# Kernel optimization log

Hardware: AMD Instinct MI355X
Metric: run time of the kernel (lower is better)

Reference implementation:

```python
import jax, jax.numpy as jnp
import numpy as np

LEVELS = 16
N_MIN = 16
N_MAX = 512
TABLE_SIZE = 524288  # 2**19, power of two -> mod == bitmask
INPUT_DIM = 2
FEATURE_DIM = 2
N_POINTS = 1048576

# geometric resolution schedule (matches torch __init__)
_b = np.exp((np.log(N_MAX) - np.log(N_MIN)) / (LEVELS - 1))
_RESOLUTIONS = np.floor(N_MIN * _b ** np.arange(LEVELS)).astype(np.float32)  # [L]
_PRIMES = np.array([1, 2654435761], dtype=np.uint32)  # first INPUT_DIM primes
# voxel corner offsets for input_dim=2 (matches _voxel_border_adds construction)
_BORDER = np.array([[0, 1, 0, 1], [0, 0, 1, 1]], dtype=np.int32)  # [D, 2**D]


def setup_inputs() -> dict:
    key = jax.random.key(0)
    kx, kt = jax.random.split(key)
    x = jax.random.uniform(kx, (N_POINTS, INPUT_DIM), dtype=jnp.float32)
    hash_tables = jax.random.normal(kt, (LEVELS, TABLE_SIZE, FEATURE_DIM), dtype=jnp.float32)
    return {"x": x, "hash_tables": hash_tables}


def reference(x, hash_tables):
    res = jnp.asarray(_RESOLUTIONS)            # [L]
    border = jnp.asarray(_BORDER)              # [D, C] with C=2**D
    primes = jnp.asarray(_PRIMES)              # [D] uint32

    # scaled coords per level: [N, D, L]
    scaled = x[:, :, None] * res[None, None, :]
    grid = jnp.floor(scaled).astype(jnp.int32)                 # [N, D, L]
    corners = grid[:, :, :, None] + border[None, :, None, :]   # [N, D, L, C]

    # spatial hash: xor of (coord * prime) per dim, mod table size.
    # uint32 arithmetic matches torch's int64 result exactly because
    # TABLE_SIZE is a power of two dividing 2**32 and coords are nonnegative.
    prod = corners.astype(jnp.uint32) * primes[None, :, None, None]  # [N, D, L, C]
    hashed = (prod[:, 0] ^ prod[:, 1]) & jnp.uint32(TABLE_SIZE - 1)  # [N, L, C]
    idx = hashed.astype(jnp.int32)

    # gather per-level features: [N, L, C, F]
    feats = hash_tables[jnp.arange(LEVELS)[None, :, None], idx]

    # interpolation weights (faithful to torch: prod over dims of |scaled - corner|)
    w = jnp.prod(jnp.abs(scaled[:, :, :, None] - corners.astype(scaled.dtype)), axis=1)  # [N, L, C]

    # sum over corners; torch output layout is [N, F, L] flattened feature-major
    out = jnp.einsum('nlc,nlcf->nfl', w, feats)  # [N, F, L]
    return out.reshape(x.shape[0], FEATURE_DIM * LEVELS)
```

## Files before the change

kernel.cpp:

```cpp
#include <hip/hip_runtime.h>
#include <stdint.h>

#define LEVELS    16
#define TSIZE     524288
#define TMASK     (TSIZE - 1)
#define PRIME1    2654435761u
#define NBINS     65536

__device__ __constant__ float c_res[LEVELS] = {
    16.f, 20.f, 25.f, 32.f, 40.f, 50.f, 64.f, 80.f,
    101.f, 128.f, 161.f, 203.f, 256.f, 322.f, 406.f, 512.f
};

__device__ __forceinline__ uint32_t morton_key(float2 p) {
    float fx = fminf(fmaxf(p.x, 0.f), 0.999999f);
    float fy = fminf(fmaxf(p.y, 0.f), 0.999999f);
    uint32_t x = (uint32_t)(fx * 256.f);
    uint32_t y = (uint32_t)(fy * 256.f);
    x = (x | (x << 4)) & 0x0F0Fu; x = (x | (x << 2)) & 0x3333u; x = (x | (x << 1)) & 0x5555u;
    y = (y | (y << 4)) & 0x0F0Fu; y = (y | (y << 2)) & 0x3333u; y = (y | (y << 1)) & 0x5555u;
    return x | (y << 1);
}

__device__ __forceinline__ void hashenc_point(float2 p, const float* __restrict__ tables,
                                              float* __restrict__ outline) {
    float acc0[LEVELS], acc1[LEVELS];
#pragma unroll
    for (int l = 0; l < LEVELS; ++l) {
        float r  = c_res[l];
        float s0 = p.x * r;
        float s1 = p.y * r;
        float g0 = floorf(s0);
        float g1 = floorf(s1);
        uint32_t i0 = (uint32_t)(int)g0;
        uint32_t i1 = (uint32_t)(int)g1;
        uint32_t hy0 = i1 * PRIME1;
        uint32_t hy1 = (i1 + 1u) * PRIME1;
        uint32_t h00 = ( i0       ^ hy0) & TMASK;
        uint32_t h10 = ((i0 + 1u) ^ hy0) & TMASK;
        uint32_t h01 = ( i0       ^ hy1) & TMASK;
        uint32_t h11 = ((i0 + 1u) ^ hy1) & TMASK;

        const float2* tab = reinterpret_cast<const float2*>(tables) + (size_t)l * TSIZE;
        float2 t00 = tab[h00];
        float2 t10 = tab[h10];
        float2 t01 = tab[h01];
        float2 t11 = tab[h11];

        float wx0 = fabsf(s0 - g0);
        float wx1 = fabsf(s0 - (g0 + 1.f));
        float wy0 = fabsf(s1 - g1);
        float wy1 = fabsf(s1 - (g1 + 1.f));
        float w00 = wx0 * wy0, w10 = wx1 * wy0, w01 = wx0 * wy1, w11 = wx1 * wy1;

        acc0[l] = w00 * t00.x + w10 * t10.x + w01 * t01.x + w11 * t11.x;
        acc1[l] = w00 * t00.y + w10 * t10.y + w01 * t01.y + w11 * t11.y;
    }
    float4* o = reinterpret_cast<float4*>(outline);
    o[0] = make_float4(acc0[0],  acc0[1],  acc0[2],  acc0[3]);
    o[1] = make_float4(acc0[4],  acc0[5],  acc0[6],  acc0[7]);
    o[2] = make_float4(acc0[8],  acc0[9],  acc0[10], acc0[11]);
    o[3] = make_float4(acc0[12], acc0[13], acc0[14], acc0[15]);
    o[4] = make_float4(acc1[0],  acc1[1],  acc1[2],  acc1[3]);
    o[5] = make_float4(acc1[4],  acc1[5],  acc1[6],  acc1[7]);
    o[6] = make_float4(acc1[8],  acc1[9],  acc1[10], acc1[11]);
    o[7] = make_float4(acc1[12], acc1[13], acc1[14], acc1[15]);
}

__global__ __launch_bounds__(256)
void zero_hist_kernel(uint32_t* __restrict__ hist) {
    hist[blockIdx.x * 256 + threadIdx.x] = 0u;
}

__global__ __launch_bounds__(256)
void hist_kernel(const float* __restrict__ x, uint32_t* __restrict__ hist, int npts) {
    int n = blockIdx.x * 256 + threadIdx.x;
    if (n >= npts) return;
    float2 p = reinterpret_cast<const float2*>(x)[n];
    atomicAdd(&hist[morton_key(p)], 1u);
}

__global__ __launch_bounds__(1024)
void scan_kernel(uint32_t* __restrict__ hist) {
    __shared__ uint32_t part[1024];
    int t = threadIdx.x;
    int base = t * 64;
    uint32_t sum = 0;
#pragma unroll 4
    for (int i = 0; i < 64; ++i) sum += hist[base + i];
    part[t] = sum;
    __syncthreads();
    for (int off = 1; off < 1024; off <<= 1) {
        uint32_t v = (t >= off) ? part[t - off] : 0u;
        __syncthreads();
        part[t] += v;
        __syncthreads();
    }
    uint32_t run = part[t] - sum;
    for (int i = 0; i < 64; ++i) {
        uint32_t old = hist[base + i];
        hist[base + i] = run;
        run += old;
    }
}

__global__ __launch_bounds__(256)
void scatter_kernel(const float* __restrict__ x, uint32_t* __restrict__ hist,
                    uint32_t* __restrict__ perm, float2* __restrict__ sx, int npts) {
    int n = blockIdx.x * 256 + threadIdx.x;
    if (n >= npts) return;
    float2 p = reinterpret_cast<const float2*>(x)[n];
    uint32_t pos = atomicAdd(&hist[morton_key(p)], 1u);
    perm[pos] = (uint32_t)n;
    sx[pos] = p;
}

__global__ __launch_bounds__(256)
void hashenc_sorted_kernel(const uint32_t* __restrict__ perm,
                           const float2* __restrict__ sx,
                           const float* __restrict__ tables,
                           float* __restrict__ out, int npts) {
    int i = blockIdx.x * 256 + threadIdx.x;
    if (i >= npts) return;
    uint32_t n = perm[i];
    float2 p = sx[i];
    hashenc_point(p, tables, out + (size_t)n * 32);
}

__global__ __launch_bounds__(256)
void hashenc_kernel(const float* __restrict__ x,
                    const float* __restrict__ tables,
                    float* __restrict__ out, int npts) {
    int n = blockIdx.x * 256 + threadIdx.x;
    if (n >= npts) return;
    float2 p = reinterpret_cast<const float2*>(x)[n];
    hashenc_point(p, tables, out + (size_t)n * 32);
}

extern "C" void kernel_launch(void* const* d_in, const int* in_sizes, int n_in,
                              void* d_out, int out_size, void* d_ws, size_t ws_size,
                              hipStream_t stream) {
    const float* x      = (const float*)d_in[0];
    const float* tables = (const float*)d_in[1];
    float* out          = (float*)d_out;
    int npts = in_sizes[0] / 2;
    int blocks = (npts + 255) / 256;

    size_t hist_bytes = (size_t)NBINS * 4;
    size_t perm_bytes = (size_t)npts * 4;
    size_t sx_bytes   = (size_t)npts * 8;
    size_t needed = hist_bytes + perm_bytes + sx_bytes;

    if (ws_size < needed) {
        hashenc_kernel<<<blocks, 256, 0, stream>>>(x, tables, out, npts);
        return;
    }

    uint32_t* hist = (uint32_t*)d_ws;
    uint32_t* perm = (uint32_t*)((char*)d_ws + hist_bytes);
    float2*   sx   = (float2*)((char*)d_ws + hist_bytes + perm_bytes);

    zero_hist_kernel<<<NBINS / 256, 256, 0, stream>>>(hist);
    hist_kernel<<<blocks, 256, 0, stream>>>(x, hist, npts);
    scan_kernel<<<1, 1024, 0, stream>>>(hist);
    scatter_kernel<<<blocks, 256, 0, stream>>>(x, hist, perm, sx, npts);
    hashenc_sorted_kernel<<<blocks, 256, 0, stream>>>(perm, sx, tables, out, npts);
}
```

Baseline: 399.6 us.

## Parallelize histogram scan across blocks and use nontemporal loads/stores in encode

Replaces the single-block serial prefix scan over 65536 bins with a two-level scan: per-chunk scans across 256 blocks, then a scan of the chunk totals. The scatter step adds the chunk offset to each bin's local position. The encoding kernel now writes its output and reads the permutation and sorted points with nontemporal hints, so streaming data does not evict hash-table lines from cache. This adds one kernel launch and relies on nontemporal semantics behaving well on this GPU.

```diff
diff --git a/kernel.cpp b/kernel.cpp
--- a/kernel.cpp
+++ b/kernel.cpp
@@ -6,6 +6,9 @@
 #define TMASK     (TSIZE - 1)
 #define PRIME1    2654435761u
 #define NBINS     65536
+#define NCHUNK    256
+
+typedef float f32x4 __attribute__((ext_vector_type(4)));
 
 __device__ __constant__ float c_res[LEVELS] = {
     16.f, 20.f, 25.f, 32.f, 40.f, 50.f, 64.f, 80.f,
@@ -56,15 +59,16 @@
         acc0[l] = w00 * t00.x + w10 * t10.x + w01 * t01.x + w11 * t11.x;
         acc1[l] = w00 * t00.y + w10 * t10.y + w01 * t01.y + w11 * t11.y;
     }
-    float4* o = reinterpret_cast<float4*>(outline);
-    o[0] = make_float4(acc0[0],  acc0[1],  acc0[2],  acc0[3]);
-    o[1] = make_float4(acc0[4],  acc0[5],  acc0[6],  acc0[7]);
-    o[2] = make_float4(acc0[8],  acc0[9],  acc0[10], acc0[11]);
-    o[3] = make_float4(acc0[12], acc0[13], acc0[14], acc0[15]);
-    o[4] = make_float4(acc1[0],  acc1[1],  acc1[2],  acc1[3]);
-    o[5] = make_float4(acc1[4],  acc1[5],  acc1[6],  acc1[7]);
-    o[6] = make_float4(acc1[8],  acc1[9],  acc1[10], acc1[11]);
-    o[7] = make_float4(acc1[12], acc1[13], acc1[14], acc1[15]);
+    f32x4* o = reinterpret_cast<f32x4*>(outline);
+    f32x4 v;
+    v = (f32x4){acc0[0],  acc0[1],  acc0[2],  acc0[3]};  __builtin_nontemporal_store(v, &o[0]);
+    v = (f32x4){acc0[4],  acc0[5],  acc0[6],  acc0[7]};  __builtin_nontemporal_store(v, &o[1]);
+    v = (f32x4){acc0[8],  acc0[9],  acc0[10], acc0[11]}; __builtin_nontemporal_store(v, &o[2]);
+    v = (f32x4){acc0[12], acc0[13], acc0[14], acc0[15]}; __builtin_nontemporal_store(v, &o[3]);
+    v = (f32x4){acc1[0],  acc1[1],  acc1[2],  acc1[3]};  __builtin_nontemporal_store(v, &o[4]);
+    v = (f32x4){acc1[4],  acc1[5],  acc1[6],  acc1[7]};  __builtin_nontemporal_store(v, &o[5]);
+    v = (f32x4){acc1[8],  acc1[9],  acc1[10], acc1[11]}; __builtin_nontemporal_store(v, &o[6]);
+    v = (f32x4){acc1[12], acc1[13], acc1[14], acc1[15]}; __builtin_nontemporal_store(v, &o[7]);
 }
 
 __global__ __launch_bounds__(256)
@@ -80,37 +84,49 @@
     atomicAdd(&hist[morton_key(p)], 1u);
 }
 
-__global__ __launch_bounds__(1024)
-void scan_kernel(uint32_t* __restrict__ hist) {
-    __shared__ uint32_t part[1024];
+__global__ __launch_bounds__(256)
+void scan1_kernel(uint32_t* __restrict__ hist, uint32_t* __restrict__ totals) {
+    __shared__ uint32_t s[NCHUNK];
     int t = threadIdx.x;
-    int base = t * 64;
-    uint32_t sum = 0;
-#pragma unroll 4
-    for (int i = 0; i < 64; ++i) sum += hist[base + i];
-    part[t] = sum;
+    int base = blockIdx.x * NCHUNK;
+    uint32_t v = hist[base + t];
+    s[t] = v;
     __syncthreads();
-    for (int off = 1; off < 1024; off <<= 1) {
-        uint32_t v = (t >= off) ? part[t - off] : 0u;
+    for (int off = 1; off < NCHUNK; off <<= 1) {
+        uint32_t u = (t >= off) ? s[t - off] : 0u;
         __syncthreads();
-        part[t] += v;
+        s[t] += u;
         __syncthreads();
     }
-    uint32_t run = part[t] - sum;
-    for (int i = 0; i < 64; ++i) {
-        uint32_t old = hist[base + i];
-        hist[base + i] = run;
-        run += old;
+    hist[base + t] = s[t] - v;
+    if (t == NCHUNK - 1) totals[blockIdx.x] = s[t];
+}
+
+__global__ __launch_bounds__(256)
+void scan2_kernel(uint32_t* __restrict__ totals) {
+    __shared__ uint32_t s[NCHUNK];
+    int t = threadIdx.x;
+    uint32_t v = totals[t];
+    s[t] = v;
+    __syncthreads();
+    for (int off = 1; off < NCHUNK; off <<= 1) {
+        uint32_t u = (t >= off) ? s[t - off] : 0u;
+        __syncthreads();
+        s[t] += u;
+        __syncthreads();
     }
+    totals[t] = s[t] - v;
 }
 
 __global__ __launch_bounds__(256)
 void scatter_kernel(const float* __restrict__ x, uint32_t* __restrict__ hist,
+                    const uint32_t* __restrict__ totals,
                     uint32_t* __restrict__ perm, float2* __restrict__ sx, int npts) {
     int n = blockIdx.x * 256 + threadIdx.x;
     if (n >= npts) return;
     float2 p = reinterpret_cast<const float2*>(x)[n];
-    uint32_t pos = atomicAdd(&hist[morton_key(p)], 1u);
+    uint32_t bin = morton_key(p);
+    uint32_t pos = totals[bin >> 8] + atomicAdd(&hist[bin], 1u);
     perm[pos] = (uint32_t)n;
     sx[pos] = p;
 }
@@ -122,8 +138,10 @@
                            float* __restrict__ out, int npts) {
     int i = blockIdx.x * 256 + threadIdx.x;
     if (i >= npts) return;
-    uint32_t n = perm[i];
-    float2 p = sx[i];
+    uint32_t n = __builtin_nontemporal_load(&perm[i]);
+    float2 p;
+    p.x = __builtin_nontemporal_load(&sx[i].x);
+    p.y = __builtin_nontemporal_load(&sx[i].y);
     hashenc_point(p, tables, out + (size_t)n * 32);
 }
 
@@ -146,23 +164,26 @@
     int npts = in_sizes[0] / 2;
     int blocks = (npts + 255) / 256;
 
-    size_t hist_bytes = (size_t)NBINS * 4;
-    size_t perm_bytes = (size_t)npts * 4;
-    size_t sx_bytes   = (size_t)npts * 8;
-    size_t needed = hist_bytes + perm_bytes + sx_bytes;
+    size_t hist_bytes   = (size_t)NBINS * 4;
+    size_t totals_bytes = (size_t)NCHUNK * 4;
+    size_t perm_bytes   = (size_t)npts * 4;
+    size_t sx_bytes     = (size_t)npts * 8;
+    size_t needed = hist_bytes + totals_bytes + perm_bytes + sx_bytes;
 
     if (ws_size < needed) {
         hashenc_kernel<<<blocks, 256, 0, stream>>>(x, tables, out, npts);
         return;
     }
 
-    uint32_t* hist = (uint32_t*)d_ws;
-    uint32_t* perm = (uint32_t*)((char*)d_ws + hist_bytes);
-    float2*   sx   = (float2*)((char*)d_ws + hist_bytes + perm_bytes);
+    uint32_t* hist   = (uint32_t*)d_ws;
+    uint32_t* totals = (uint32_t*)((char*)d_ws + hist_bytes);
+    uint32_t* perm   = (uint32_t*)((char*)d_ws + hist_bytes + totals_bytes);
+    float2*   sx     = (float2*)((char*)d_ws + hist_bytes + totals_bytes + perm_bytes);
 
     zero_hist_kernel<<<NBINS / 256, 256, 0, stream>>>(hist);
     hist_kernel<<<blocks, 256, 0, stream>>>(x, hist, npts);
-    scan_kernel<<<1, 1024, 0, stream>>>(hist);
-    scatter_kernel<<<blocks, 256, 0, stream>>>(x, hist, perm, sx, npts);
+    scan1_kernel<<<NBINS / NCHUNK, 256, 0, stream>>>(hist, totals);
+    scan2_kernel<<<1, 256, 0, stream>>>(totals);
+    scatter_kernel<<<blocks, 256, 0, stream>>>(x, hist, totals, perm, sx, npts);
     hashenc_sorted_kernel<<<blocks, 256, 0, stream>>>(perm, sx, tables, out, npts);
 }
```

Result: slower. 502.2 us (+25.7%).
